# Performance work log

Measured on AMD Instinct MI355X. Metric: run time of the kernel, lower is better.

The kernel has to match this reference:

```python
import jax, jax.numpy as jnp
import numpy as np

N_EMBED = 8192
EMBED_DIM = 4
BETA = 0.25


def setup_inputs() -> dict:
    key = jax.random.key(0)
    k1, k2 = jax.random.split(key)
    z = jax.random.normal(k1, (8, EMBED_DIM, 64, 64), dtype=jnp.float32)
    # torch init: uniform(-1/n_embed, 1/n_embed)
    embed_w = jax.random.uniform(k2, (N_EMBED, EMBED_DIM), dtype=jnp.float32,
                                 minval=-1.0 / N_EMBED, maxval=1.0 / N_EMBED)
    return {"z": z, "embed_w": embed_w}


def reference(z, embed_w):
    # z: [B, C, H, W] -> [B, H, W, C]
    z_nhwc = jnp.transpose(z, (0, 2, 3, 1))
    z_flat = z_nhwc.reshape(-1, EMBED_DIM)  # [N, D]
    # squared L2 distances: ||z||^2 + ||e||^2 - 2 z e^T  -> [N, n_embed]
    d = (jnp.sum(z_flat * z_flat, axis=1, keepdims=True)
         + jnp.sum(embed_w * embed_w, axis=1)
         - 2.0 * z_flat @ embed_w.T)
    min_idx = jnp.argmin(d, axis=1)  # [N] int
    z_q = embed_w[min_idx].reshape(z_nhwc.shape)  # [B, H, W, C]
    sg = jax.lax.stop_gradient
    loss = (jnp.mean((sg(z_q) - z_nhwc) ** 2)
            + BETA * jnp.mean((z_q - sg(z_nhwc)) ** 2))
    # straight-through estimator
    z_q_ste = z_nhwc + sg(z_q - z_nhwc)
    z_q_out = jnp.transpose(z_q_ste, (0, 3, 1, 2))  # back to [B, C, H, W]
    return z_q_out, loss, min_idx
```

## Files before the change

kernel.cpp:

```cpp
#include <hip/hip_runtime.h>
#include <math.h>

typedef float v2f __attribute__((ext_vector_type(2)));

#define N_POINTS 32768
#define NUM_EMBED 8192
#define NPAIRS 4096
#define CH 64
#define CPC (NUM_EMBED / CH)
#define PAIRS (NPAIRS / CH)
#define PPT 8
#define RB 512
#define CSTRIDE 4096

__global__ void vq_prep_kernel(const float4* __restrict__ E, v2f* __restrict__ Epk) {
    int p = blockIdx.x * 256 + threadIdx.x;
    if (p < NPAIRS) {
        float4 a = E[2 * p];
        float4 b = E[2 * p + 1];
        Epk[4 * p + 0] = (v2f){a.x, b.x};
        Epk[4 * p + 1] = (v2f){a.y, b.y};
        Epk[4 * p + 2] = (v2f){a.z, b.z};
        Epk[4 * p + 3] = (v2f){a.w, b.w};
    }
}

__device__ __forceinline__ v2f pk_mul(v2f a, v2f b) {
    v2f d; asm("v_pk_mul_f32 %0, %1, %2" : "=v"(d) : "v"(a), "v"(b)); return d;
}
__device__ __forceinline__ v2f pk_fma(v2f a, v2f b, v2f c) {
    v2f d; asm("v_pk_fma_f32 %0, %1, %2, %3" : "=v"(d) : "v"(a), "v"(b), "v"(c)); return d;
}

__device__ __forceinline__ unsigned int fkey(float f) {
    unsigned int b = __float_as_uint(f);
    return b ^ (0x80000000u | (unsigned int)((int)b >> 31));
}

__global__ __launch_bounds__(256) void vq_filter_kernel(
        const float* __restrict__ z, const v2f* __restrict__ Epk,
        float* __restrict__ cmax) {
    __shared__ alignas(16) v2f sE[PAIRS * 4];

    const int c = blockIdx.y;
    if (threadIdx.x < PAIRS * 2) {
        ((float4*)sE)[threadIdx.x] =
            ((const float4*)(Epk + (size_t)c * PAIRS * 4))[threadIdx.x];
    }

    const int n0 = blockIdx.x * (256 * PPT) + threadIdx.x;

    v2f zv[PPT][4];
    #pragma unroll
    for (int p = 0; p < PPT; ++p) {
        int n = n0 + p * 256;
        int b = n >> 12, hw = n & 4095;
        const float* zp = z + b * 16384 + hw;
        zv[p][0] = (v2f){zp[0], zp[0]};
        zv[p][1] = (v2f){zp[CSTRIDE], zp[CSTRIDE]};
        zv[p][2] = (v2f){zp[2 * CSTRIDE], zp[2 * CSTRIDE]};
        zv[p][3] = (v2f){zp[3 * CSTRIDE], zp[3 * CSTRIDE]};
    }

    __syncthreads();

    float run[PPT];
    #pragma unroll
    for (int p = 0; p < PPT; ++p) run[p] = -__builtin_inff();

    const float4* sE4 = (const float4*)sE;
    #pragma unroll 2
    for (int t = 0; t < PAIRS; ++t) {
        float4 E01 = sE4[2 * t];
        float4 E23 = sE4[2 * t + 1];
        v2f e0 = {E01.x, E01.y};
        v2f e1 = {E01.z, E01.w};
        v2f e2 = {E23.x, E23.y};
        v2f e3 = {E23.z, E23.w};
        #pragma unroll
        for (int p = 0; p < PPT; ++p) {
            v2f dot = pk_mul(zv[p][0], e0);
            dot = pk_fma(zv[p][1], e1, dot);
            dot = pk_fma(zv[p][2], e2, dot);
            dot = pk_fma(zv[p][3], e3, dot);
            run[p] = fmaxf(fmaxf(dot.x, dot.y), run[p]);
        }
    }

    #pragma unroll
    for (int p = 0; p < PPT; ++p)
        cmax[c * N_POINTS + n0 + p * 256] = run[p];
}

__global__ __launch_bounds__(RB) void vq_resolve_kernel(
        const float* __restrict__ z, const float4* __restrict__ E,
        const float* __restrict__ cmax,
        float* __restrict__ out, double* __restrict__ partial) {
    __shared__ double sdata[RB / 64];
    const int lane = threadIdx.x & 63;
    const int wid = threadIdx.x >> 6;
    const int n = blockIdx.x * (RB / 64) + wid;

    const int b = n >> 12;
    const int hw = n & 4095;
    const float* zp = z + b * 16384 + hw;
    float z0 = zp[0];
    float z1 = zp[CSTRIDE];
    float z2 = zp[2 * CSTRIDE];
    float z3 = zp[3 * CSTRIDE];
    float zz = __fmul_rn(z0, z0);
    zz = __fadd_rn(zz, __fmul_rn(z1, z1));
    zz = __fadd_rn(zz, __fmul_rn(z2, z2));
    zz = __fadd_rn(zz, __fmul_rn(z3, z3));

    float cm = cmax[lane * N_POINTS + n];
    float gmax = cm;
    #pragma unroll
    for (int off = 32; off; off >>= 1)
        gmax = fmaxf(gmax, __shfl_xor(gmax, off));

    float u = __fmul_rn(__fadd_rn(zz, 0.01f), 2.38418579e-07f);
    float thr = __fsub_rn(gmax, __fadd_rn(__fadd_rn(u, u), 1e-7f));
    unsigned long long mask = __ballot(cm >= thr);

    unsigned long long bkey = ~0ull;
    while (mask) {
        int c = __builtin_ctzll(mask);
        mask &= mask - 1ull;
        int j0 = c * CPC + lane;
        #pragma unroll
        for (int h = 0; h < 2; ++h) {
            int j = j0 + h * 64;
            float4 e = E[j];
            float ee = __fmul_rn(e.x, e.x);
            ee = __fadd_rn(ee, __fmul_rn(e.y, e.y));
            ee = __fadd_rn(ee, __fmul_rn(e.z, e.z));
            ee = __fadd_rn(ee, __fmul_rn(e.w, e.w));
            float dot = __fmul_rn(z0, e.x);
            dot = __fmaf_rn(z1, e.y, dot);
            dot = __fmaf_rn(z2, e.z, dot);
            dot = __fmaf_rn(z3, e.w, dot);
            float d = __fmaf_rn(-2.0f, dot, __fadd_rn(zz, ee));
            unsigned long long key =
                ((unsigned long long)fkey(d) << 32) | (unsigned int)j;
            bkey = key < bkey ? key : bkey;
        }
    }
    #pragma unroll
    for (int off = 32; off; off >>= 1) {
        unsigned long long o = __shfl_xor(bkey, off);
        bkey = o < bkey ? o : bkey;
    }
    int besti = (int)(unsigned int)(bkey & 0xFFFFFFFFull);

    if (lane == 0) {
        float4 e = E[besti];
        float* op = out + b * 16384 + hw;
        float t0 = __fsub_rn(e.x, z0);
        float t1 = __fsub_rn(e.y, z1);
        float t2 = __fsub_rn(e.z, z2);
        float t3 = __fsub_rn(e.w, z3);
        op[0]           = __fadd_rn(z0, t0);
        op[CSTRIDE]     = __fadd_rn(z1, t1);
        op[2 * CSTRIDE] = __fadd_rn(z2, t2);
        op[3 * CSTRIDE] = __fadd_rn(z3, t3);
        out[131073 + n] = (float)besti;
        double ds = (double)__fmul_rn(t0, t0) + (double)__fmul_rn(t1, t1)
                  + (double)__fmul_rn(t2, t2) + (double)__fmul_rn(t3, t3);
        sdata[wid] = ds;
    }
    __syncthreads();
    if (threadIdx.x == 0) {
        double s = 0.0;
        #pragma unroll
        for (int w = 0; w < RB / 64; ++w) s += sdata[w];
        partial[blockIdx.x] = s;
    }
}

__global__ void vq_loss_kernel(const double* __restrict__ partial, float* __restrict__ out) {
    __shared__ double sdata[256];
    int t = threadIdx.x;
    double s = 0.0;
    for (int i = t; i < 4096; i += 256) s += partial[i];
    sdata[t] = s;
    __syncthreads();
    #pragma unroll
    for (int st = 128; st > 0; st >>= 1) {
        if (t < st) sdata[t] += sdata[t + st];
        __syncthreads();
    }
    if (t == 0) {
        float m = (float)(sdata[0] / 131072.0);
        out[131072] = __fadd_rn(m, __fmul_rn(0.25f, m));
    }
}

extern "C" void kernel_launch(void* const* d_in, const int* in_sizes, int n_in,
                              void* d_out, int out_size, void* d_ws, size_t ws_size,
                              hipStream_t stream) {
    const float* z = (const float*)d_in[0];
    const float4* E = (const float4*)d_in[1];
    float* out = (float*)d_out;

    char* ws = (char*)d_ws;
    v2f* Epk = (v2f*)ws;
    float* cmaxb = (float*)(ws + 131072);
    double* partial = (double*)(ws + 131072 + (size_t)CH * N_POINTS * 4);

    vq_prep_kernel<<<NPAIRS / 256, 256, 0, stream>>>(E, Epk);
    vq_filter_kernel<<<dim3(N_POINTS / (256 * PPT), CH), 256, 0, stream>>>(z, Epk, cmaxb);
    vq_resolve_kernel<<<N_POINTS / (RB / 64), RB, 0, stream>>>(z, E, cmaxb, out, partial);
    vq_loss_kernel<<<1, 256, 0, stream>>>(partial, out);
}
```

Before: 58.11 us.

## Process eight codebook chunks per filter block and store chunk maxima point-major

The filter kernel now handles 8 codebook chunks per block with 2 points per thread, instead of one chunk with 8 points per thread. It writes the per-chunk maxima in a point-major [N, 64] layout using float4 stores. The resolve kernel then reads the 64 chunk maxima for a point contiguously rather than with a large stride. The trade-off is more shared-memory traffic per FMA, since each thread reuses each loaded codebook entry across only 2 points, plus 8 running maxima per point held in registers.

Result: slower. 61.42 us (+5.7%).

```diff
diff --git a/kernel.cpp b/kernel.cpp
--- a/kernel.cpp
+++ b/kernel.cpp
@@ -9,7 +9,8 @@
 #define CH 64
 #define CPC (NUM_EMBED / CH)
 #define PAIRS (NPAIRS / CH)
-#define PPT 8
+#define CPB 8
+#define FPPT 2
 #define RB 512
 #define CSTRIDE 4096
 
@@ -40,19 +41,22 @@
 __global__ __launch_bounds__(256) void vq_filter_kernel(
         const float* __restrict__ z, const v2f* __restrict__ Epk,
         float* __restrict__ cmax) {
-    __shared__ alignas(16) v2f sE[PAIRS * 4];
-
-    const int c = blockIdx.y;
-    if (threadIdx.x < PAIRS * 2) {
-        ((float4*)sE)[threadIdx.x] =
-            ((const float4*)(Epk + (size_t)c * PAIRS * 4))[threadIdx.x];
-    }
-
-    const int n0 = blockIdx.x * (256 * PPT) + threadIdx.x;
-
-    v2f zv[PPT][4];
-    #pragma unroll
-    for (int p = 0; p < PPT; ++p) {
+    __shared__ alignas(16) float4 sE4[CPB * PAIRS * 2];
+
+    const int cbase = blockIdx.y * CPB;
+
+    {
+        const float4* gE = (const float4*)(Epk + (size_t)cbase * PAIRS * 4);
+        #pragma unroll
+        for (int i = 0; i < (CPB * PAIRS * 2) / 256; ++i)
+            sE4[i * 256 + threadIdx.x] = gE[i * 256 + threadIdx.x];
+    }
+
+    const int n0 = blockIdx.x * (256 * FPPT) + threadIdx.x;
+
+    v2f zv[FPPT][4];
+    #pragma unroll
+    for (int p = 0; p < FPPT; ++p) {
         int n = n0 + p * 256;
         int b = n >> 12, hw = n & 4095;
         const float* zp = z + b * 16384 + hw;
@@ -64,32 +68,40 @@
 
     __syncthreads();
 
-    float run[PPT];
-    #pragma unroll
-    for (int p = 0; p < PPT; ++p) run[p] = -__builtin_inff();
-
-    const float4* sE4 = (const float4*)sE;
+    float run[FPPT][CPB];
+    #pragma unroll
+    for (int p = 0; p < FPPT; ++p)
+        #pragma unroll
+        for (int k = 0; k < CPB; ++k) run[p][k] = -__builtin_inff();
+
     #pragma unroll 2
     for (int t = 0; t < PAIRS; ++t) {
-        float4 E01 = sE4[2 * t];
-        float4 E23 = sE4[2 * t + 1];
-        v2f e0 = {E01.x, E01.y};
-        v2f e1 = {E01.z, E01.w};
-        v2f e2 = {E23.x, E23.y};
-        v2f e3 = {E23.z, E23.w};
-        #pragma unroll
-        for (int p = 0; p < PPT; ++p) {
-            v2f dot = pk_mul(zv[p][0], e0);
-            dot = pk_fma(zv[p][1], e1, dot);
-            dot = pk_fma(zv[p][2], e2, dot);
-            dot = pk_fma(zv[p][3], e3, dot);
-            run[p] = fmaxf(fmaxf(dot.x, dot.y), run[p]);
+        #pragma unroll
+        for (int k = 0; k < CPB; ++k) {
+            float4 E01 = sE4[k * 128 + 2 * t];
+            float4 E23 = sE4[k * 128 + 2 * t + 1];
+            v2f e0 = {E01.x, E01.y};
+            v2f e1 = {E01.z, E01.w};
+            v2f e2 = {E23.x, E23.y};
+            v2f e3 = {E23.z, E23.w};
+            #pragma unroll
+            for (int p = 0; p < FPPT; ++p) {
+                v2f dot = pk_mul(zv[p][0], e0);
+                dot = pk_fma(zv[p][1], e1, dot);
+                dot = pk_fma(zv[p][2], e2, dot);
+                dot = pk_fma(zv[p][3], e3, dot);
+                run[p][k] = fmaxf(fmaxf(dot.x, dot.y), run[p][k]);
+            }
         }
     }
 
     #pragma unroll
-    for (int p = 0; p < PPT; ++p)
-        cmax[c * N_POINTS + n0 + p * 256] = run[p];
+    for (int p = 0; p < FPPT; ++p) {
+        int n = n0 + p * 256;
+        float4* dst = (float4*)(cmax + (size_t)n * CH + cbase);
+        dst[0] = make_float4(run[p][0], run[p][1], run[p][2], run[p][3]);
+        dst[1] = make_float4(run[p][4], run[p][5], run[p][6], run[p][7]);
+    }
 }
 
 __global__ __launch_bounds__(RB) void vq_resolve_kernel(
@@ -113,7 +125,7 @@
     zz = __fadd_rn(zz, __fmul_rn(z2, z2));
     zz = __fadd_rn(zz, __fmul_rn(z3, z3));
 
-    float cm = cmax[lane * N_POINTS + n];
+    float cm = cmax[(size_t)n * CH + lane];
     float gmax = cm;
     #pragma unroll
     for (int off = 32; off; off >>= 1)
@@ -209,7 +221,7 @@
     double* partial = (double*)(ws + 131072 + (size_t)CH * N_POINTS * 4);
 
     vq_prep_kernel<<<NPAIRS / 256, 256, 0, stream>>>(E, Epk);
-    vq_filter_kernel<<<dim3(N_POINTS / (256 * PPT), CH), 256, 0, stream>>>(z, Epk, cmaxb);
+    vq_filter_kernel<<<dim3(N_POINTS / (256 * FPPT), CH / CPB), 256, 0, stream>>>(z, Epk, cmaxb);
     vq_resolve_kernel<<<N_POINTS / (RB / 64), RB, 0, stream>>>(z, E, cmaxb, out, partial);
     vq_loss_kernel<<<1, 256, 0, stream>>>(partial, out);
 }
```
